# Kernel tuning notes

Measured on AMD Instinct MI355X. Metric: run time of the kernel, lower is better.

Reference implementation:

```python
import jax, jax.numpy as jnp
import numpy as np

K = 3  # kernel_size
P = 1  # padding (must satisfy K == 2*P+1 for the original einsum to be shape-valid)


def setup_inputs() -> dict:
    key = jax.random.key(0)
    k1, k2, k3 = jax.random.split(key, 3)
    b, i, c, L, o = 16, 64, 4, 4096, 64
    x = jax.random.normal(k1, (b, i, c, L), dtype=jnp.float32)
    time_tensor = jax.random.uniform(k2, (b, c, L), dtype=jnp.float32)
    weights = jax.random.normal(k3, (o, i, c, K), dtype=jnp.float32)
    return {"x": x, "time_tensor": time_tensor, "weights": weights}


def reference(x, time_tensor, weights):
    """x: (b,i,c,L), time_tensor: (b,c,L), weights: (o,i,c,K) -> (b,o,c,L).

    Faithful to the torch module: pad x/time by P on the time axis, unfold x
    into sliding windows, pad the unfolded tensor again by P, multiply by the
    time scalar per (b,c,l) and contract over (i,k), then crop P from each end.
    The time factor is scalar per output element, so we factor it out of the
    einsum instead of materializing the (b,o,i,c,k,l) dynamic_weights tensor --
    mathematically identical, massively cheaper.
    """
    xp = jnp.pad(x, ((0, 0), (0, 0), (0, 0), (P, P)))            # (b,i,c,L+2P)
    tp = jnp.pad(time_tensor, ((0, 0), (0, 0), (P, P)))          # (b,c,L+2P)
    Lw = xp.shape[-1] - K + 1                                    # == L since K=2P+1
    # unfold -> (b,i,c,K,Lw), matching torch's permute(0,2,1,4,3) after transpose
    xu = jnp.stack([xp[..., j:j + Lw] for j in range(K)], axis=-2)
    xu = jnp.transpose(xu, (0, 2, 1, 3, 4))                      # (b,c,i,K,Lw)
    xu = jnp.pad(xu, ((0, 0), (0, 0), (0, 0), (0, 0), (P, P)))   # (b,c,i,K,Lw+2P)
    conv = jnp.einsum('oick,bcikl->bocl', weights, xu)           # (b,o,c,L+2P)
    out = conv * tp[:, None, :, :]
    return out[..., P:-P]                                        # (b,o,c,L)
```

## Files before the change

### kernel.cpp

```cpp
#include <hip/hip_runtime.h>


#define NB 16
#define NI 64
#define NC 4
#define NL 4096
#define NO 64
#define KW 3
#define LT 64
#define NCH 4
#define LBLK (LT * NCH)
#define ROWS (LBLK + 2)
#define ROWB 128
#define LDSB (ROWS * ROWB)

#define W_PACK_BYTES (NO * NI * NC * KW * 2)

typedef float f32x4 __attribute__((ext_vector_type(4)));
typedef short bf16x8 __attribute__((ext_vector_type(8)));
typedef unsigned int u32x2 __attribute__((ext_vector_type(2)));

__device__ inline unsigned short f2bf(float f) {
    unsigned int u = __builtin_bit_cast(unsigned int, f);
    u += 0x7FFFu + ((u >> 16) & 1u);
    return (unsigned short)(u >> 16);
}

__device__ __forceinline__ void block_sync_lds() {
    asm volatile("s_waitcnt lgkmcnt(0)" ::: "memory");
    __builtin_amdgcn_s_barrier();
    asm volatile("" ::: "memory");
}

__global__ __launch_bounds__(256)
void prepack_w_kernel(const float* __restrict__ w, unsigned short* __restrict__ wp) {
    const int idx = blockIdx.x * 256 + threadIdx.x;
    const float v = w[idx];
    const int k = idx % 3;
    int r = idx / 3;
    const int c = r & 3;  r >>= 2;
    const int i = r & 63;
    const int o = r >> 6;
    const int cc   = k * 2 + (i >> 5);
    const int lane = (((i >> 3) & 3) << 4) | (o & 15);
    const int j    = i & 7;
    const int wv   = o >> 4;
    wp[(((c * 4 + wv) * 6 + cc) * 64 + lane) * 8 + j] = f2bf(v);
}

__device__ __forceinline__ void stage_load(const float* __restrict__ xb,
                                           int l0, int g, f32x4 s[4]) {
    const float* p = xb + (size_t)(4 * g) * (NC * NL) + l0;
    s[0] = *(const f32x4*)(p);
    s[1] = *(const f32x4*)(p + NC * NL);
    s[2] = *(const f32x4*)(p + 2 * NC * NL);
    s[3] = *(const f32x4*)(p + 3 * NC * NL);
}

__device__ __forceinline__ void stage_write(char* __restrict__ lds,
                                            int r0, int g, const f32x4 s[4]) {
#pragma unroll
    for (int r = 0; r < 4; ++r) {
        const int rr = r0 + r;
        u32x2 pk;
        pk[0] = (unsigned int)f2bf(s[0][r]) | ((unsigned int)f2bf(s[1][r]) << 16);
        pk[1] = (unsigned int)f2bf(s[2][r]) | ((unsigned int)f2bf(s[3][r]) << 16);
        *(u32x2*)(lds + rr * ROWB + ((8 * g) ^ ((rr & 7) << 4))) = pk;
    }
}

__global__ __launch_bounds__(256, 4)
void tconv_mfma_kernel(const float* __restrict__ x,
                       const float* __restrict__ tt,
                       const unsigned short* __restrict__ wp,
                       float* __restrict__ out)
{
    __shared__ char lds[LDSB];

    const int t    = threadIdx.x;
    const int lane = t & 63;
    const int wave = t >> 6;
    const int c    = blockIdx.y;
    const int b    = blockIdx.z;
    const int lb0  = blockIdx.x * LBLK;
    const int g    = wave * 4 + (lane >> 4);
    const int lq   = 4 * (lane & 15);

    const float* xb = x + ((size_t)b * NI * NC + c) * NL;
    const float* tb = tt + (size_t)(b * NC + c) * NL;

    f32x4 s[4][4];
#pragma unroll
    for (int ch = 0; ch < NCH; ++ch)
        stage_load(xb, lb0 + ch * LT + lq, g, s[ch]);
    float h = 0.f; int hrow = 0, hcol = 0;
    if (t < 128) {
        const int which = t & 1;
        const int i     = t >> 1;
        hrow = which ? (LBLK + 1) : 0;
        hcol = 2 * i;
        const int lh = which ? (lb0 + LBLK) : (lb0 - 1);
        if (lh >= 0 && lh < NL) h = xb[(size_t)i * (NC * NL) + lh];
    }

#pragma unroll
    for (int ch = 0; ch < NCH; ++ch)
        stage_write(lds, 1 + ch * LT + lq, g, s[ch]);
    if (t < 128)
        *(unsigned short*)(lds + hrow * ROWB + (hcol ^ ((hrow & 7) << 4))) = f2bf(h);

    block_sync_lds();

    const int lcol  = lane & 15;
    const int ksub2 = (lane >> 4) * 16;
    const int rbase = wave * LT;
    const int lwave = lb0 + wave * LT;

#pragma unroll
    for (int hh = 0; hh < 2; ++hh) {
        bf16x8 wfrag[2][6];
        {
            const bf16x8* wpb = (const bf16x8*)wp
                + (size_t)((c * 4 + 2 * hh) * 6) * 64 + lane;
#pragma unroll
            for (int s2 = 0; s2 < 2; ++s2)
#pragma unroll
                for (int cc = 0; cc < 6; ++cc)
                    wfrag[s2][cc] = wpb[(s2 * 6 + cc) * 64];
        }
#pragma unroll
        for (int lt = 0; lt < 4; ++lt) {
            const int l0 = lwave + lt * 16 + (lane >> 4) * 4;
            const f32x4 tv = *(const f32x4*)(tb + l0);
            f32x4 acc[2] = {};
#pragma unroll
            for (int cc = 0; cc < 6; ++cc) {
                const int k   = cc >> 1;
                const int ih  = cc & 1;
                const int row = rbase + lt * 16 + lcol + k;
                const int off = row * ROWB + ((ih * 64 + ksub2) ^ ((row & 7) << 4));
                const bf16x8 xf = *(const bf16x8*)(lds + off);
                acc[0] = __builtin_amdgcn_mfma_f32_16x16x32_bf16(xf, wfrag[0][cc], acc[0], 0, 0, 0);
                acc[1] = __builtin_amdgcn_mfma_f32_16x16x32_bf16(xf, wfrag[1][cc], acc[1], 0, 0, 0);
            }
#pragma unroll
            for (int s2 = 0; s2 < 2; ++s2) {
                const int o = (2 * hh + s2) * 16 + lcol;
                float* os = out + ((size_t)b * NO * NC + (size_t)o * NC + c) * NL;
                f32x4 r;
#pragma unroll
                for (int q = 0; q < 4; ++q) r[q] = acc[s2][q] * tv[q];
                *(f32x4*)(os + l0) = r;
            }
        }
    }
}

extern "C" void kernel_launch(void* const* d_in, const int* in_sizes, int n_in,
                              void* d_out, int out_size, void* d_ws, size_t ws_size,
                              hipStream_t stream) {
    const float* x  = (const float*)d_in[0];
    const float* tt = (const float*)d_in[1];
    const float* w  = (const float*)d_in[2];
    float* out = (float*)d_out;
    unsigned short* wpck = (unsigned short*)d_ws;

    prepack_w_kernel<<<dim3(NO * NI * NC * KW / 256), dim3(256), 0, stream>>>(w, wpck);

    dim3 grid(NL / LBLK, NC, NB);
    tconv_mfma_kernel<<<grid, dim3(256), 0, stream>>>(x, tt, wpck, out);
}
```

Measured before the change: 34.90 us.

## Pipeline x staging across chunks with register double-buffering and per-wave output channels

Restructures the main kernel so that each block streams eight 32-wide chunks of the time axis. Global loads for chunk n+2 are issued while chunk n is computed, then written to LDS behind a barrier. Work is also reassigned so each wave owns 16 output channels across all positions and keeps a single set of weight fragments, instead of each wave owning a position slice and reloading weights for two output halves. The aim is to hide global-load latency and cut register pressure, at the cost of a block barrier per chunk and smaller load granularity.

```diff
diff --git a/kernel.cpp b/kernel.cpp
--- a/kernel.cpp
+++ b/kernel.cpp
@@ -7,8 +7,8 @@
 #define NL 4096
 #define NO 64
 #define KW 3
-#define LT 64
-#define NCH 4
+#define LT 32
+#define NCH 8
 #define LBLK (LT * NCH)
 #define ROWS (LBLK + 2)
 #define ROWB 128
@@ -18,7 +18,6 @@
 
 typedef float f32x4 __attribute__((ext_vector_type(4)));
 typedef short bf16x8 __attribute__((ext_vector_type(8)));
-typedef unsigned int u32x2 __attribute__((ext_vector_type(2)));
 
 __device__ inline unsigned short f2bf(float f) {
     unsigned int u = __builtin_bit_cast(unsigned int, f);
@@ -49,23 +48,47 @@
 }
 
 __device__ __forceinline__ void stage_load(const float* __restrict__ xb,
-                                           int l0, int g, f32x4 s[4]) {
-    const float* p = xb + (size_t)(4 * g) * (NC * NL) + l0;
+                                           int l0q, int g2, f32x4 s[2]) {
+    const float* p = xb + (size_t)(2 * g2) * (NC * NL) + l0q;
     s[0] = *(const f32x4*)(p);
     s[1] = *(const f32x4*)(p + NC * NL);
-    s[2] = *(const f32x4*)(p + 2 * NC * NL);
-    s[3] = *(const f32x4*)(p + 3 * NC * NL);
 }
 
 __device__ __forceinline__ void stage_write(char* __restrict__ lds,
-                                            int r0, int g, const f32x4 s[4]) {
+                                            int ch, int q, int g2,
+                                            const f32x4 s[2]) {
 #pragma unroll
     for (int r = 0; r < 4; ++r) {
-        const int rr = r0 + r;
-        u32x2 pk;
-        pk[0] = (unsigned int)f2bf(s[0][r]) | ((unsigned int)f2bf(s[1][r]) << 16);
-        pk[1] = (unsigned int)f2bf(s[2][r]) | ((unsigned int)f2bf(s[3][r]) << 16);
-        *(u32x2*)(lds + rr * ROWB + ((8 * g) ^ ((rr & 7) << 4))) = pk;
+        const int row = ch * LT + 4 * q + r + 1;
+        const unsigned int pk =
+            (unsigned int)f2bf(s[0][r]) | ((unsigned int)f2bf(s[1][r]) << 16);
+        *(unsigned int*)(lds + row * ROWB + ((4 * g2) ^ ((row & 7) << 4))) = pk;
+    }
+}
+
+__device__ __forceinline__ void compute_chunk(const char* __restrict__ lds,
+                                              const bf16x8 wfrag[6],
+                                              const float* __restrict__ tb,
+                                              float* __restrict__ ob,
+                                              int ch, int lb0, int lane) {
+    const int lcol  = lane & 15;
+    const int ksub2 = (lane >> 4) * 16;
+#pragma unroll
+    for (int lt = 0; lt < 2; ++lt) {
+        const int l0 = lb0 + ch * LT + lt * 16 + (lane >> 4) * 4;
+        const f32x4 tv = *(const f32x4*)(tb + l0);
+        f32x4 acc = {};
+#pragma unroll
+        for (int cc = 0; cc < 6; ++cc) {
+            const int row = ch * LT + lt * 16 + lcol + (cc >> 1);
+            const int off = row * ROWB + ((((cc & 1) << 6) + ksub2) ^ ((row & 7) << 4));
+            const bf16x8 xf = *(const bf16x8*)(lds + off);
+            acc = __builtin_amdgcn_mfma_f32_16x16x32_bf16(xf, wfrag[cc], acc, 0, 0, 0);
+        }
+        f32x4 r;
+#pragma unroll
+        for (int qq = 0; qq < 4; ++qq) r[qq] = acc[qq] * tv[qq];
+        *(f32x4*)(ob + l0) = r;
     }
 }
 
@@ -83,16 +106,18 @@
     const int c    = blockIdx.y;
     const int b    = blockIdx.z;
     const int lb0  = blockIdx.x * LBLK;
-    const int g    = wave * 4 + (lane >> 4);
-    const int lq   = 4 * (lane & 15);
+    const int g2   = t >> 3;
+    const int q    = t & 7;
+    const int lq   = 4 * q;
 
     const float* xb = x + ((size_t)b * NI * NC + c) * NL;
     const float* tb = tt + (size_t)(b * NC + c) * NL;
+    float* ob = out + ((size_t)b * NO * NC
+                       + (size_t)(wave * 16 + (lane & 15)) * NC + c) * NL;
 
-    f32x4 s[4][4];
-#pragma unroll
-    for (int ch = 0; ch < NCH; ++ch)
-        stage_load(xb, lb0 + ch * LT + lq, g, s[ch]);
+    f32x4 sA[2], sB[2];
+    stage_load(xb, lb0 + 0 * LT + lq, g2, sA);
+    stage_load(xb, lb0 + 1 * LT + lq, g2, sB);
     float h = 0.f; int hrow = 0, hcol = 0;
     if (t < 128) {
         const int which = t & 1;
@@ -103,57 +128,35 @@
         if (lh >= 0 && lh < NL) h = xb[(size_t)i * (NC * NL) + lh];
     }
 
+    bf16x8 wfrag[6];
+    {
+        const bf16x8* wpb = (const bf16x8*)wp + (size_t)((c * 4 + wave) * 6) * 64 + lane;
 #pragma unroll
-    for (int ch = 0; ch < NCH; ++ch)
-        stage_write(lds, 1 + ch * LT + lq, g, s[ch]);
+        for (int cc = 0; cc < 6; ++cc) wfrag[cc] = wpb[cc * 64];
+    }
+
+    stage_write(lds, 0, q, g2, sA);
+    stage_write(lds, 1, q, g2, sB);
     if (t < 128)
         *(unsigned short*)(lds + hrow * ROWB + (hcol ^ ((hrow & 7) << 4))) = f2bf(h);
-
     block_sync_lds();
 
-    const int lcol  = lane & 15;
-    const int ksub2 = (lane >> 4) * 16;
-    const int rbase = wave * LT;
-    const int lwave = lb0 + wave * LT;
+#pragma unroll
+    for (int cn = 0; cn < NCH - 2; ++cn) {
+        if ((cn & 1) == 0) {
+            stage_load(xb, lb0 + (cn + 2) * LT + lq, g2, sA);
+            compute_chunk(lds, wfrag, tb, ob, cn, lb0, lane);
+            stage_write(lds, cn + 2, q, g2, sA);
+        } else {
+            stage_load(xb, lb0 + (cn + 2) * LT + lq, g2, sB);
+            compute_chunk(lds, wfrag, tb, ob, cn, lb0, lane);
+            stage_write(lds, cn + 2, q, g2, sB);
+        }
+        block_sync_lds();
+    }
 
-#pragma unroll
-    for (int hh = 0; hh < 2; ++hh) {
-        bf16x8 wfrag[2][6];
-        {
-            const bf16x8* wpb = (const bf16x8*)wp
-                + (size_t)((c * 4 + 2 * hh) * 6) * 64 + lane;
-#pragma unroll
-            for (int s2 = 0; s2 < 2; ++s2)
-#pragma unroll
-                for (int cc = 0; cc < 6; ++cc)
-                    wfrag[s2][cc] = wpb[(s2 * 6 + cc) * 64];
-        }
-#pragma unroll
-        for (int lt = 0; lt < 4; ++lt) {
-            const int l0 = lwave + lt * 16 + (lane >> 4) * 4;
-            const f32x4 tv = *(const f32x4*)(tb + l0);
-            f32x4 acc[2] = {};
-#pragma unroll
-            for (int cc = 0; cc < 6; ++cc) {
-                const int k   = cc >> 1;
-                const int ih  = cc & 1;
-                const int row = rbase + lt * 16 + lcol + k;
-                const int off = row * ROWB + ((ih * 64 + ksub2) ^ ((row & 7) << 4));
-                const bf16x8 xf = *(const bf16x8*)(lds + off);
-                acc[0] = __builtin_amdgcn_mfma_f32_16x16x32_bf16(xf, wfrag[0][cc], acc[0], 0, 0, 0);
-                acc[1] = __builtin_amdgcn_mfma_f32_16x16x32_bf16(xf, wfrag[1][cc], acc[1], 0, 0, 0);
-            }
-#pragma unroll
-            for (int s2 = 0; s2 < 2; ++s2) {
-                const int o = (2 * hh + s2) * 16 + lcol;
-                float* os = out + ((size_t)b * NO * NC + (size_t)o * NC + c) * NL;
-                f32x4 r;
-#pragma unroll
-                for (int q = 0; q < 4; ++q) r[q] = acc[s2][q] * tv[q];
-                *(f32x4*)(os + l0) = r;
-            }
-        }
-    }
+    compute_chunk(lds, wfrag, tb, ob, NCH - 2, lb0, lane);
+    compute_chunk(lds, wfrag, tb, ob, NCH - 1, lb0, lane);
 }
 
 extern "C" void kernel_launch(void* const* d_in, const int* in_sizes, int n_in,
```

After: 33.01 us (median of 3 runs). -5.4%, faster.
